# Optimization experiments

Measured on AMD Instinct MI355X. Metric: run time of the kernel, lower is better.

## Reference

```python
import jax, jax.numpy as jnp
import numpy as np
import math

D_MODEL = 1024
N_HEADS = 16
D_HEAD = D_MODEL // N_HEADS


def layer_norm(x, gamma, beta, eps=1e-5):
    mu = jnp.mean(x, axis=-1, keepdims=True)
    var = jnp.var(x, axis=-1, keepdims=True)
    return (x - mu) / jnp.sqrt(var + eps) * gamma + beta


def setup_inputs() -> dict:
    key = jax.random.key(0)
    ks = jax.random.split(key, 12)
    B, T, d = 4, 2048, D_MODEL
    s = 0.02
    x = jax.random.normal(ks[0], (B, T, d), dtype=jnp.float32)
    t = jnp.arange(B * T, dtype=jnp.float32).reshape(B, T) % T  # continuous positions
    return {
        "x": x,
        "t": t,
        "w_qkv": jax.random.normal(ks[1], (d, 3 * d), dtype=jnp.float32) * s,
        "b_qkv": jnp.zeros((3 * d,), jnp.float32),
        "w_proj": jax.random.normal(ks[2], (d, d), dtype=jnp.float32) * s,
        "b_proj": jnp.zeros((d,), jnp.float32),
        "g1": jnp.ones((d,), jnp.float32),
        "beta1": jnp.zeros((d,), jnp.float32),
        "g2": jnp.ones((d,), jnp.float32),
        "beta2": jnp.zeros((d,), jnp.float32),
        "w_mlp1": jax.random.normal(ks[3], (d, 4 * d), dtype=jnp.float32) * s,
        "b_mlp1": jnp.zeros((4 * d,), jnp.float32),
        "w_mlp2": jax.random.normal(ks[4], (4 * d, d), dtype=jnp.float32) * s,
        "b_mlp2": jnp.zeros((d,), jnp.float32),
    }


def reference(x, t, w_qkv, b_qkv, w_proj, b_proj, g1, beta1, g2, beta2, w_mlp1, b_mlp1, w_mlp2, b_mlp2):
    B, T, d = x.shape
    H, dh = N_HEADS, D_HEAD
    scale = dh ** -0.5

    h = layer_norm(x, g1, beta1)
    qkv = h @ w_qkv + b_qkv  # [B,T,3d]
    q, k, v = jnp.split(qkv, 3, axis=-1)
    # [B,T,H,dh] -> [B,H,T,dh]
    q = q.reshape(B, T, H, dh).transpose(0, 2, 1, 3)
    k = k.reshape(B, T, H, dh).transpose(0, 2, 1, 3)
    v = v.reshape(B, T, H, dh).transpose(0, 2, 1, 3)

    # ContinuousRoPE on d_head
    half = dh // 2
    freqs = jnp.exp(jnp.arange(half, dtype=jnp.float32) * (-math.log(10000.0) / (half - 1)))
    args = t[:, :, None] * freqs  # [B,T,half]
    cos = jnp.tile(jnp.cos(args), (1, 1, 2))[:, None]  # [B,1,T,dh]
    sin = jnp.tile(jnp.sin(args), (1, 1, 2))[:, None]

    def rotate_half(u):
        u1, u2 = u[..., :dh // 2], u[..., dh // 2:]
        return jnp.concatenate((-u2, u1), axis=-1)

    q = q * cos + rotate_half(q) * sin
    k = k * cos + rotate_half(k) * sin

    attn = jnp.einsum("bhqd,bhkd->bhqk", q, k) * scale  # [B,H,T,T]
    causal = jnp.tril(jnp.ones((T, T), dtype=bool))
    attn = jnp.where(causal, attn, -jnp.inf)
    attn = jax.nn.softmax(attn, axis=-1)
    o = jnp.einsum("bhqk,bhkd->bhqd", attn, v)  # [B,H,T,dh]
    o = o.transpose(0, 2, 1, 3).reshape(B, T, d)

    x1 = o @ w_proj + b_proj + x
    h2 = layer_norm(x1, g2, beta2)
    mlp = jax.nn.gelu(h2 @ w_mlp1 + b_mlp1, approximate=False) @ w_mlp2 + b_mlp2
    return x1 + mlp
```

## Files before the change

kernel.cpp:

```cpp
#include <hip/hip_runtime.h>

typedef __bf16  bf16x8 __attribute__((ext_vector_type(8)));
typedef float   f32x4  __attribute__((ext_vector_type(4)));

typedef const __attribute__((address_space(1))) void* gas_p;
typedef __attribute__((address_space(3))) void*       las_p;

__device__ __forceinline__ void glds16(const void* g, void* l) {
  __builtin_amdgcn_global_load_lds((gas_p)g, (las_p)l, 16, 0, 0);
}

__device__ __forceinline__ ushort f2bf(float f) {
  unsigned u = __float_as_uint(f);
  u += 0x7fffu + ((u >> 16) & 1u);
  return (ushort)(u >> 16);
}

__global__ __launch_bounds__(256) void castT_k(const float* __restrict__ w,
                                               ushort* __restrict__ wT,
                                               const int Kd, const int Nd) {
  __shared__ float t[32][33];
  const int nb = blockIdx.x * 32, kb = blockIdx.y * 32;
  const int tx = threadIdx.x & 31, ty = threadIdx.x >> 5;
#pragma unroll
  for (int r = 0; r < 32; r += 8)
    t[ty + r][tx] = w[(size_t)(kb + ty + r) * Nd + nb + tx];
  __syncthreads();
#pragma unroll
  for (int r = 0; r < 32; r += 8)
    wT[(size_t)(nb + ty + r) * Kd + kb + tx] = f2bf(t[tx][ty + r]);
}

__global__ __launch_bounds__(256) void ln_k(const float* __restrict__ x,
                                            const float* __restrict__ gam,
                                            const float* __restrict__ bet,
                                            ushort* __restrict__ out) {
  const int row = blockIdx.x, tid = threadIdx.x;
  const float4 v = ((const float4*)(x + (size_t)row * 1024))[tid];
  float s  = v.x + v.y + v.z + v.w;
  float sq = v.x * v.x + v.y * v.y + v.z * v.z + v.w * v.w;
#pragma unroll
  for (int o = 32; o > 0; o >>= 1) { s += __shfl_xor(s, o); sq += __shfl_xor(sq, o); }
  __shared__ float red[8];
  const int wid = tid >> 6, lane = tid & 63;
  if (lane == 0) { red[wid] = s; red[4 + wid] = sq; }
  __syncthreads();
  s  = red[0] + red[1] + red[2] + red[3];
  sq = red[4] + red[5] + red[6] + red[7];
  const float mu   = s * (1.0f / 1024.0f);
  const float var  = sq * (1.0f / 1024.0f) - mu * mu;
  const float rstd = rsqrtf(var + 1e-5f);
  const float4 gv = ((const float4*)gam)[tid];
  const float4 bv = ((const float4*)bet)[tid];
  ushort4 o4;
  o4.x = f2bf((v.x - mu) * rstd * gv.x + bv.x);
  o4.y = f2bf((v.y - mu) * rstd * gv.y + bv.y);
  o4.z = f2bf((v.z - mu) * rstd * gv.z + bv.z);
  o4.w = f2bf((v.w - mu) * rstd * gv.w + bv.w);
  ((ushort4*)(out + (size_t)row * 1024))[tid] = o4;
}

__global__ __launch_bounds__(256) void vtrans_k(const ushort* __restrict__ Vn,
                                                ushort* __restrict__ Vt) {
  const int bh = blockIdx.y, i0 = blockIdx.x * 64, tid = threadIdx.x;
  __shared__ ushort t[64][65];
  const ushort* src = Vn + (size_t)bh * (2048 * 64);
#pragma unroll
  for (int kk = 0; kk < 16; ++kk) {
    const int e = tid + kk * 256, r = e >> 6, c = e & 63;
    t[r][c] = src[(size_t)(i0 + r) * 64 + c];
  }
  __syncthreads();
  ushort* dst = Vt + (size_t)bh * (64 * 2048);
#pragma unroll
  for (int kk = 0; kk < 16; ++kk) {
    const int e = tid + kk * 256, r = e >> 6, c = e & 63;
    dst[(size_t)r * 2048 + i0 + c] = t[c][r];
  }
}

template <int EPI>
__global__ __launch_bounds__(256) void gemm_k(
    const ushort* __restrict__ A, const ushort* __restrict__ Bt,
    const int M, const int N, const int K,
    const float* __restrict__ bias,
    const float* __restrict__ resid,
    float* __restrict__ outf,
    ushort* __restrict__ outb,
    ushort* __restrict__ qo, ushort* __restrict__ ko, ushort* __restrict__ vo) {
  __shared__ ushort lA[2][128 * 32];
  __shared__ ushort lB[2][128 * 32];
  const int tid = threadIdx.x;
  const int wid = tid >> 6, lane = tid & 63;
  const int l15 = lane & 15, g = lane >> 4;
  const int m0 = blockIdx.y * 128, n0 = blockIdx.x * 128;
  const int wm = wid >> 1, wn = wid & 1;

  const int srow = wid * 16 + (lane >> 2);
  const int scol = (lane & 3) * 8;
  const ushort* Ag0 = A + (size_t)(m0 + srow) * K + scol;
  const ushort* Ag1 = Ag0 + (size_t)64 * K;
  const ushort* Bg0 = Bt + (size_t)(n0 + srow) * K + scol;
  const ushort* Bg1 = Bg0 + (size_t)64 * K;

  f32x4 acc[4][4] = {};

  const int nk = K >> 5;
  int cur = 0;
  glds16(Ag0, &lA[0][wid * 512]);
  glds16(Ag1, &lA[0][(wid + 4) * 512]);
  glds16(Bg0, &lB[0][wid * 512]);
  glds16(Bg1, &lB[0][(wid + 4) * 512]);

  for (int t = 0; t < nk; ++t) {
    __syncthreads();
    if (t + 1 < nk) {
      const int kt = (t + 1) << 5;
      const int nb = cur ^ 1;
      glds16(Ag0 + kt, &lA[nb][wid * 512]);
      glds16(Ag1 + kt, &lA[nb][(wid + 4) * 512]);
      glds16(Bg0 + kt, &lB[nb][wid * 512]);
      glds16(Bg1 + kt, &lB[nb][(wid + 4) * 512]);
    }
    const ushort* lar = &lA[cur][(wm * 64 + l15) * 32 + g * 8];
    const ushort* lbr = &lB[cur][(wn * 64 + l15) * 32 + g * 8];
    bf16x8 af[4], bfr[4];
#pragma unroll
    for (int m = 0; m < 4; ++m) af[m] = *(const bf16x8*)(lar + m * 16 * 32);
#pragma unroll
    for (int n = 0; n < 4; ++n) bfr[n] = *(const bf16x8*)(lbr + n * 16 * 32);
#pragma unroll
    for (int m = 0; m < 4; ++m)
#pragma unroll
      for (int n = 0; n < 4; ++n)
        acc[m][n] = __builtin_amdgcn_mfma_f32_16x16x32_bf16(af[m], bfr[n], acc[m][n], 0, 0, 0);
    cur ^= 1;
  }

  const int rb = m0 + wm * 64;
  const int cb = n0 + wn * 64;
  if constexpr (EPI == 0) {
#pragma unroll
    for (int m = 0; m < 4; ++m)
#pragma unroll
      for (int r = 0; r < 4; ++r) {
        const int s = rb + m * 16 + g * 4 + r;
        const int bb = s >> 11, ii = s & 2047;
#pragma unroll
        for (int n = 0; n < 2; ++n) {
          const int c = cb + n * 16 + l15;
          const int which = c >> 10, h = (c >> 6) & 15, dd = c & 63;
          const float vlo = acc[m][n][r] + bias[c];
          const float vhi = acc[m][n + 2][r] + bias[c + 32];
          const size_t off = ((size_t)((bb * 16 + h) * 2048 + ii)) * 64;
          if (which == 2) {
            vo[off + dd]      = f2bf(vlo);
            vo[off + dd + 32] = f2bf(vhi);
          } else {
            const float fr = __expf(-0.29710776f * (float)dd);
            const float ang = (float)ii * fr;
            const float c0 = cosf(ang), s0 = sinf(ang);
            float rlo = vlo * c0 - vhi * s0;
            float rhi = vhi * c0 + vlo * s0;
            if (which == 0) { rlo *= 0.125f; rhi *= 0.125f; }
            ushort* dst = (which == 0) ? qo : ko;
            dst[off + dd]      = f2bf(rlo);
            dst[off + dd + 32] = f2bf(rhi);
          }
        }
      }
  } else {
#pragma unroll
    for (int m = 0; m < 4; ++m)
#pragma unroll
      for (int n = 0; n < 4; ++n)
#pragma unroll
        for (int r = 0; r < 4; ++r) {
          const int row = rb + m * 16 + g * 4 + r;
          const int col = cb + n * 16 + l15;
          float v = acc[m][n][r] + bias[col];
          if constexpr (EPI == 1) {
            v += resid[(size_t)row * N + col];
            outf[(size_t)row * N + col] = v;
          } else {
            const float ge = 0.5f * v * (1.0f + erff(v * 0.70710678f));
            outb[(size_t)row * N + col] = f2bf(ge);
          }
        }
  }
}

__global__ __launch_bounds__(256) void attn_k(const ushort* __restrict__ Q,
                                              const ushort* __restrict__ K,
                                              const ushort* __restrict__ Vt,
                                              ushort* __restrict__ O) {
  const int bh = blockIdx.x;
  const int qt = 31 - blockIdx.y;
  const int tid = threadIdx.x, wid = tid >> 6, lane = tid & 63;
  const int l15 = lane & 15, g = lane >> 4;
  const size_t bho = (size_t)bh * (2048 * 64);
  const ushort* Qb = Q + bho;
  const char*   KbB = (const char*)(K + bho);
  const char*   VbB = (const char*)(Vt + bho);
  const int b = bh >> 4, h = bh & 15;

  __shared__ ushort kl[2][64 * 64];
  __shared__ ushort vl[2][64 * 64];
  __shared__ ushort pl[4][16 * 64];

  const int rbase = wid * 16;
  const int rsub  = lane >> 3;
  const int cbyte = (lane & 7) << 4;
  const int scb   = cbyte ^ (rsub << 4);

  const int q0 = qt * 64 + wid * 16;

  const bf16x8 qf0 = *(const bf16x8*)&Qb[(size_t)(q0 + l15) * 64 + g * 8];
  const bf16x8 qf1 = *(const bf16x8*)&Qb[(size_t)(q0 + l15) * 64 + 32 + g * 8];

  f32x4 o[4] = {};
  float m = -1e30f, l = 0.f;

  char* pbase = (char*)pl[wid];
  const int swz  = (l15 & 7) << 4;
  const int skey = (l15 & 7) << 4;

  const int nkt = qt + 1;

  {
    const char* ks0 = KbB + (size_t)(0 + rbase + rsub) * 128 + scb;
    const char* vs0 = VbB + (size_t)(rbase + rsub) * 4096 + scb;
    glds16(ks0,            (char*)kl[0] + rbase * 128);
    glds16(ks0 + 8 * 128,  (char*)kl[0] + (rbase + 8) * 128);
    glds16(vs0,            (char*)vl[0] + rbase * 128);
    glds16(vs0 + 8 * 4096, (char*)vl[0] + (rbase + 8) * 128);
  }
  int cur = 0;

  for (int kt = 0; kt < nkt; ++kt) {
    const int k0 = kt * 64;
    __syncthreads();
    if (kt + 1 < nkt) {
      const int nb = cur ^ 1, k1 = k0 + 64;
      const char* ks0 = KbB + (size_t)(k1 + rbase + rsub) * 128 + scb;
      const char* vs0 = VbB + (size_t)(rbase + rsub) * 4096 + (size_t)k1 * 2 + scb;
      glds16(ks0,            (char*)kl[nb] + rbase * 128);
      glds16(ks0 + 8 * 128,  (char*)kl[nb] + (rbase + 8) * 128);
      glds16(vs0,            (char*)vl[nb] + rbase * 128);
      glds16(vs0 + 8 * 4096, (char*)vl[nb] + (rbase + 8) * 128);
    }
    const char* Klds = (const char*)kl[cur];
    const char* Vlds = (const char*)vl[cur];

    f32x4 st[4];
    __builtin_amdgcn_s_setprio(1);
#pragma unroll
    for (int sub = 0; sub < 4; ++sub) {
      const int kr = sub * 16 + l15;
      const bf16x8 kf0 = *(const bf16x8*)(Klds + kr * 128 + ((g * 16) ^ skey));
      const bf16x8 kf1 = *(const bf16x8*)(Klds + kr * 128 + ((64 + g * 16) ^ skey));
      f32x4 z = {0.f, 0.f, 0.f, 0.f};
      f32x4 sv = __builtin_amdgcn_mfma_f32_16x16x32_bf16(kf0, qf0, z, 0, 0, 0);
      sv = __builtin_amdgcn_mfma_f32_16x16x32_bf16(kf1, qf1, sv, 0, 0, 0);
      st[sub] = sv;
    }
    __builtin_amdgcn_s_setprio(0);
    if (k0 + 63 > q0) {
#pragma unroll
      for (int sub = 0; sub < 4; ++sub) {
        const int kk = k0 + sub * 16 + g * 4;
#pragma unroll
        for (int r = 0; r < 4; ++r)
          if (kk + r > q0 + l15) st[sub][r] = -1e30f;
      }
    }
    f32x4 mv = st[0];
#pragma unroll
    for (int sub = 1; sub < 4; ++sub)
#pragma unroll
      for (int r = 0; r < 4; ++r) mv[r] = fmaxf(mv[r], st[sub][r]);
    float tm = fmaxf(fmaxf(mv[0], mv[1]), fmaxf(mv[2], mv[3]));
    tm = fmaxf(tm, __shfl_xor(tm, 16));
    tm = fmaxf(tm, __shfl_xor(tm, 32));
    if (!__all(tm - m <= 8.0f)) {
      const float mnew = fmaxf(m, tm);
      const float corr = __expf(m - mnew);
      m = mnew;
      l *= corr;
      float cr[4];
#pragma unroll
      for (int r = 0; r < 4; ++r) cr[r] = __shfl(corr, g * 4 + r);
#pragma unroll
      for (int nf = 0; nf < 4; ++nf)
#pragma unroll
        for (int r = 0; r < 4; ++r) o[nf][r] *= cr[r];
    }
    float ps = 0.f;
#pragma unroll
    for (int sub = 0; sub < 4; ++sub) {
      const float p0 = __expf(st[sub][0] - m);
      const float p1 = __expf(st[sub][1] - m);
      const float p2 = __expf(st[sub][2] - m);
      const float p3 = __expf(st[sub][3] - m);
      ps += (p0 + p1) + (p2 + p3);
      ushort4 pk;
      pk.x = f2bf(p0); pk.y = f2bf(p1); pk.z = f2bf(p2); pk.w = f2bf(p3);
      *(ushort4*)(pbase + ((l15 * 128 + ((sub * 32 + g * 8) ^ swz)))) = pk;
    }
    ps += __shfl_xor(ps, 16);
    ps += __shfl_xor(ps, 32);
    l += ps;
    const bf16x8 pf0 = *(const bf16x8*)(pbase + (l15 * 128 + ((g * 16) ^ swz)));
    const bf16x8 pf1 = *(const bf16x8*)(pbase + (l15 * 128 + ((64 + g * 16) ^ swz)));
    __builtin_amdgcn_s_setprio(1);
#pragma unroll
    for (int nf = 0; nf < 4; ++nf) {
      const int dr = nf * 16 + l15;
      const bf16x8 vf0 = *(const bf16x8*)(Vlds + dr * 128 + ((g * 16) ^ skey));
      const bf16x8 vf1 = *(const bf16x8*)(Vlds + dr * 128 + ((64 + g * 16) ^ skey));
      o[nf] = __builtin_amdgcn_mfma_f32_16x16x32_bf16(pf0, vf0, o[nf], 0, 0, 0);
      o[nf] = __builtin_amdgcn_mfma_f32_16x16x32_bf16(pf1, vf1, o[nf], 0, 0, 0);
    }
    __builtin_amdgcn_s_setprio(0);
    cur ^= 1;
  }
  const float linv = 1.0f / l;
  float li[4];
#pragma unroll
  for (int r = 0; r < 4; ++r) li[r] = __shfl(linv, g * 4 + r);
#pragma unroll
  for (int nf = 0; nf < 4; ++nf)
#pragma unroll
    for (int r = 0; r < 4; ++r) {
      const int qr = q0 + g * 4 + r;
      O[((size_t)(b * 2048 + qr)) * 1024 + h * 64 + nf * 16 + l15] = f2bf(o[nf][r] * li[r]);
    }
}

extern "C" void kernel_launch(void* const* d_in, const int* in_sizes, int n_in,
                              void* d_out, int out_size, void* d_ws, size_t ws_size,
                              hipStream_t stream) {
  const float* x      = (const float*)d_in[0];
  const float* w_qkv  = (const float*)d_in[2];
  const float* b_qkv  = (const float*)d_in[3];
  const float* w_proj = (const float*)d_in[4];
  const float* b_proj = (const float*)d_in[5];
  const float* g1     = (const float*)d_in[6];
  const float* be1    = (const float*)d_in[7];
  const float* g2     = (const float*)d_in[8];
  const float* be2    = (const float*)d_in[9];
  const float* w_mlp1 = (const float*)d_in[10];
  const float* b_mlp1 = (const float*)d_in[11];
  const float* w_mlp2 = (const float*)d_in[12];
  const float* b_mlp2 = (const float*)d_in[13];

  char* ws = (char*)d_ws;
  ushort* WQKVT  = (ushort*)(ws + 0);
  ushort* WPROJT = (ushort*)(ws + 6291456);
  ushort* WMLP1T = (ushort*)(ws + 8388608);
  ushort* WMLP2T = (ushort*)(ws + 16777216);
  ushort* H      = (ushort*)(ws + 25165824);
  ushort* Qs     = (ushort*)(ws + 41943040);
  ushort* Ks     = (ushort*)(ws + 58720256);
  ushort* Vn     = (ushort*)(ws + 75497472);
  ushort* Vt     = (ushort*)(ws + 92274688);
  ushort* M1     = (ushort*)(ws + 41943040);
  float*  X1     = (float*)(ws + 109051904);

  castT_k<<<dim3(3072 / 32, 1024 / 32), 256, 0, stream>>>(w_qkv, WQKVT, 1024, 3072);
  castT_k<<<dim3(1024 / 32, 1024 / 32), 256, 0, stream>>>(w_proj, WPROJT, 1024, 1024);
  castT_k<<<dim3(4096 / 32, 1024 / 32), 256, 0, stream>>>(w_mlp1, WMLP1T, 1024, 4096);
  castT_k<<<dim3(1024 / 32, 4096 / 32), 256, 0, stream>>>(w_mlp2, WMLP2T, 4096, 1024);

  ln_k<<<8192, 256, 0, stream>>>(x, g1, be1, H);

  gemm_k<0><<<dim3(3072 / 128, 8192 / 128), 256, 0, stream>>>(
      H, WQKVT, 8192, 3072, 1024, b_qkv, nullptr, nullptr, nullptr, Qs, Ks, Vn);

  vtrans_k<<<dim3(32, 64), 256, 0, stream>>>(Vn, Vt);

  attn_k<<<dim3(64, 32), 256, 0, stream>>>(Qs, Ks, Vt, H );

  gemm_k<1><<<dim3(1024 / 128, 8192 / 128), 256, 0, stream>>>(
      H, WPROJT, 8192, 1024, 1024, b_proj, x, X1, nullptr, nullptr, nullptr, nullptr);

  ln_k<<<8192, 256, 0, stream>>>(X1, g2, be2, H );

  gemm_k<2><<<dim3(4096 / 128, 8192 / 128), 256, 0, stream>>>(
      H, WMLP1T, 8192, 4096, 1024, b_mlp1, nullptr, nullptr, M1, nullptr, nullptr, nullptr);

  gemm_k<1><<<dim3(1024 / 128, 8192 / 128), 256, 0, stream>>>(
      M1, WMLP2T, 8192, 1024, 4096, b_mlp2, X1, (float*)d_out, nullptr, nullptr, nullptr, nullptr);
}
```

Measured before the change: 569.9 us.

## Replace GEMM with 256-wide tiled, 8-wave, swizzled, finer-pipelined kernel

```diff
diff --git a/kernel.cpp b/kernel.cpp
--- a/kernel.cpp
+++ b/kernel.cpp
@@ -15,6 +15,13 @@
   u += 0x7fffu + ((u >> 16) & 1u);
   return (ushort)(u >> 16);
 }
+
+__device__ __forceinline__ void barx() {
+  asm volatile("" ::: "memory");
+  __builtin_amdgcn_s_barrier();
+  asm volatile("" ::: "memory");
+}
+#define WAITVM(N) asm volatile("s_waitcnt vmcnt(" #N ")" ::: "memory")
 
 __global__ __launch_bounds__(256) void castT_k(const float* __restrict__ w,
                                                ushort* __restrict__ wT,
@@ -79,8 +86,8 @@
   }
 }
 
-template <int EPI>
-__global__ __launch_bounds__(256) void gemm_k(
+template <int MF, int EPI>
+__global__ __launch_bounds__(512, 2) void gemm2_k(
     const ushort* __restrict__ A, const ushort* __restrict__ Bt,
     const int M, const int N, const int K,
     const float* __restrict__ bias,
@@ -88,60 +95,104 @@
     float* __restrict__ outf,
     ushort* __restrict__ outb,
     ushort* __restrict__ qo, ushort* __restrict__ ko, ushort* __restrict__ vo) {
-  __shared__ ushort lA[2][128 * 32];
-  __shared__ ushort lB[2][128 * 32];
-  const int tid = threadIdx.x;
-  const int wid = tid >> 6, lane = tid & 63;
+  constexpr int BM = MF * 32;
+  constexpr int GA = MF / 4;
+  extern __shared__ ushort lds_u[];
+  ushort* aL = lds_u;
+  ushort* bL = lds_u + 4 * BM * 32;
+
+  const int tid = threadIdx.x, wid = tid >> 6, lane = tid & 63;
   const int l15 = lane & 15, g = lane >> 4;
-  const int m0 = blockIdx.y * 128, n0 = blockIdx.x * 128;
-  const int wm = wid >> 1, wn = wid & 1;
-
-  const int srow = wid * 16 + (lane >> 2);
-  const int scol = (lane & 3) * 8;
-  const ushort* Ag0 = A + (size_t)(m0 + srow) * K + scol;
-  const ushort* Ag1 = Ag0 + (size_t)64 * K;
-  const ushort* Bg0 = Bt + (size_t)(n0 + srow) * K + scol;
-  const ushort* Bg1 = Bg0 + (size_t)64 * K;
-
-  f32x4 acc[4][4] = {};
-
-  const int nk = K >> 5;
+  const int wr = wid >> 2, wc = wid & 3;
+  const int m0 = blockIdx.y * BM, n0 = blockIdx.x * 256;
+
+  const int srl = lane >> 2;
+  const int scb = ((lane & 3) << 4) ^ (((lane >> 3) & 3) << 4);
+  const int rk  = ((l15 >> 1) & 3) << 4;
+  const size_t Krow = (size_t)K * 2;
+
+  auto stageA = [&](int b, int kh, int t) {
+#pragma unroll
+    for (int L = 0; L < GA; ++L) {
+      const char* src = (const char*)A + (size_t)(m0 + L * 128 + wid * 16 + srl) * Krow
+                        + (size_t)t * 128 + kh * 64 + scb;
+      glds16(src, (char*)aL + (size_t)((b * 2 + kh) * BM + L * 128 + wid * 16) * 64);
+    }
+  };
+  auto stageB = [&](int b, int kh, int t) {
+#pragma unroll
+    for (int L = 0; L < 2; ++L) {
+      const char* src = (const char*)Bt + (size_t)(n0 + L * 128 + wid * 16 + srl) * Krow
+                        + (size_t)t * 128 + kh * 64 + scb;
+      glds16(src, (char*)bL + (size_t)((b * 2 + kh) * 256 + L * 128 + wid * 16) * 64);
+    }
+  };
+
+  bf16x8 af[MF], bfr[4];
+  f32x4 acc[MF][4] = {};
+
+  auto loadA = [&](int b, int kh) {
+#pragma unroll
+    for (int m = 0; m < MF; ++m)
+      af[m] = *(const bf16x8*)((const char*)aL +
+          (size_t)((b * 2 + kh) * BM + wr * (BM / 2) + m * 16 + l15) * 64 + ((g * 16) ^ rk));
+  };
+  auto loadB = [&](int b, int kh, int nh) {
+#pragma unroll
+    for (int n = 0; n < 2; ++n)
+      bfr[nh * 2 + n] = *(const bf16x8*)((const char*)bL +
+          (size_t)((b * 2 + kh) * 256 + wc * 64 + (nh * 2 + n) * 16 + l15) * 64 + ((g * 16) ^ rk));
+  };
+  auto mfma8 = [&](int nh) {
+    __builtin_amdgcn_s_setprio(1);
+#pragma unroll
+    for (int m = 0; m < MF; ++m) {
+      acc[m][nh * 2]     = __builtin_amdgcn_mfma_f32_16x16x32_bf16(af[m], bfr[nh * 2],     acc[m][nh * 2],     0, 0, 0);
+      acc[m][nh * 2 + 1] = __builtin_amdgcn_mfma_f32_16x16x32_bf16(af[m], bfr[nh * 2 + 1], acc[m][nh * 2 + 1], 0, 0, 0);
+    }
+    __builtin_amdgcn_s_setprio(0);
+  };
+
+  stageA(0, 0, 0); stageB(0, 0, 0); stageA(0, 1, 0); stageB(0, 1, 0);
+  if constexpr (MF == 8) { WAITVM(4); } else { WAITVM(3); }
+  barx();
+
+  const int nk = K >> 6;
   int cur = 0;
-  glds16(Ag0, &lA[0][wid * 512]);
-  glds16(Ag1, &lA[0][(wid + 4) * 512]);
-  glds16(Bg0, &lB[0][wid * 512]);
-  glds16(Bg1, &lB[0][(wid + 4) * 512]);
-
   for (int t = 0; t < nk; ++t) {
-    __syncthreads();
-    if (t + 1 < nk) {
-      const int kt = (t + 1) << 5;
-      const int nb = cur ^ 1;
-      glds16(Ag0 + kt, &lA[nb][wid * 512]);
-      glds16(Ag1 + kt, &lA[nb][(wid + 4) * 512]);
-      glds16(Bg0 + kt, &lB[nb][wid * 512]);
-      glds16(Bg1 + kt, &lB[nb][(wid + 4) * 512]);
-    }
-    const ushort* lar = &lA[cur][(wm * 64 + l15) * 32 + g * 8];
-    const ushort* lbr = &lB[cur][(wn * 64 + l15) * 32 + g * 8];
-    bf16x8 af[4], bfr[4];
-#pragma unroll
-    for (int m = 0; m < 4; ++m) af[m] = *(const bf16x8*)(lar + m * 16 * 32);
-#pragma unroll
-    for (int n = 0; n < 4; ++n) bfr[n] = *(const bf16x8*)(lbr + n * 16 * 32);
-#pragma unroll
-    for (int m = 0; m < 4; ++m)
-#pragma unroll
-      for (int n = 0; n < 4; ++n)
-        acc[m][n] = __builtin_amdgcn_mfma_f32_16x16x32_bf16(af[m], bfr[n], acc[m][n], 0, 0, 0);
-    cur ^= 1;
-  }
-
-  const int rb = m0 + wm * 64;
-  const int cb = n0 + wn * 64;
+    const bool pf = (t + 1 < nk);
+    const int nb = cur ^ 1;
+    loadA(cur, 0); loadB(cur, 0, 0);
+    if (pf) stageA(nb, 0, t + 1);
+    barx();
+    mfma8(0);
+    barx();
+    loadB(cur, 0, 1);
+    if (pf) stageB(nb, 0, t + 1);
+    barx();
+    mfma8(1);
+    if (pf) { if constexpr (MF == 8) { WAITVM(4); } else { WAITVM(3); } }
+    else    { WAITVM(0); }
+    barx();
+    loadA(cur, 1); loadB(cur, 1, 0);
+    if (pf) stageA(nb, 1, t + 1);
+    barx();
+    mfma8(0);
+    barx();
+    loadB(cur, 1, 1);
+    if (pf) stageB(nb, 1, t + 1);
+    barx();
+    mfma8(1);
+    if (pf) { if constexpr (MF == 8) { WAITVM(4); } else { WAITVM(3); } }
+    barx();
+    cur = nb;
+  }
+
+  const int rb = m0 + wr * (BM / 2);
+  const int cb = n0 + wc * 64;
   if constexpr (EPI == 0) {
 #pragma unroll
-    for (int m = 0; m < 4; ++m)
+    for (int m = 0; m < MF; ++m)
 #pragma unroll
       for (int r = 0; r < 4; ++r) {
         const int s = rb + m * 16 + g * 4 + r;
@@ -171,7 +222,7 @@
       }
   } else {
 #pragma unroll
-    for (int m = 0; m < 4; ++m)
+    for (int m = 0; m < MF; ++m)
 #pragma unroll
       for (int n = 0; n < 4; ++n)
 #pragma unroll
@@ -226,7 +277,6 @@
   const int skey = (l15 & 7) << 4;
 
   const int nkt = qt + 1;
-
   {
     const char* ks0 = KbB + (size_t)(0 + rbase + rsub) * 128 + scb;
     const char* vs0 = VbB + (size_t)(rbase + rsub) * 4096 + scb;
@@ -367,6 +417,10 @@
   ushort* M1     = (ushort*)(ws + 41943040);
   float*  X1     = (float*)(ws + 109051904);
 
+  hipFuncSetAttribute((const void*)gemm2_k<8, 0>, hipFuncAttributeMaxDynamicSharedMemorySize, 131072);
+  hipFuncSetAttribute((const void*)gemm2_k<8, 2>, hipFuncAttributeMaxDynamicSharedMemorySize, 131072);
+  hipFuncSetAttribute((const void*)gemm2_k<4, 1>, hipFuncAttributeMaxDynamicSharedMemorySize, 98304);
+
   castT_k<<<dim3(3072 / 32, 1024 / 32), 256, 0, stream>>>(w_qkv, WQKVT, 1024, 3072);
   castT_k<<<dim3(1024 / 32, 1024 / 32), 256, 0, stream>>>(w_proj, WPROJT, 1024, 1024);
   castT_k<<<dim3(4096 / 32, 1024 / 32), 256, 0, stream>>>(w_mlp1, WMLP1T, 1024, 4096);
@@ -374,21 +428,21 @@
 
   ln_k<<<8192, 256, 0, stream>>>(x, g1, be1, H);
 
-  gemm_k<0><<<dim3(3072 / 128, 8192 / 128), 256, 0, stream>>>(
+  gemm2_k<8, 0><<<dim3(3072 / 256, 8192 / 256), 512, 131072, stream>>>(
       H, WQKVT, 8192, 3072, 1024, b_qkv, nullptr, nullptr, nullptr, Qs, Ks, Vn);
 
   vtrans_k<<<dim3(32, 64), 256, 0, stream>>>(Vn, Vt);
 
   attn_k<<<dim3(64, 32), 256, 0, stream>>>(Qs, Ks, Vt, H );
 
-  gemm_k<1><<<dim3(1024 / 128, 8192 / 128), 256, 0, stream>>>(
+  gemm2_k<4, 1><<<dim3(1024 / 256, 8192 / 128), 512, 98304, stream>>>(
       H, WPROJT, 8192, 1024, 1024, b_proj, x, X1, nullptr, nullptr, nullptr, nullptr);
 
   ln_k<<<8192, 256, 0, stream>>>(X1, g2, be2, H );
 
-  gemm_k<2><<<dim3(4096 / 128, 8192 / 128), 256, 0, stream>>>(
+  gemm2_k<8, 2><<<dim3(4096 / 256, 8192 / 256), 512, 131072, stream>>>(
       H, WMLP1T, 8192, 4096, 1024, b_mlp1, nullptr, nullptr, M1, nullptr, nullptr, nullptr);
 
-  gemm_k<1><<<dim3(1024 / 128, 8192 / 128), 256, 0, stream>>>(
+  gemm2_k<4, 1><<<dim3(1024 / 256, 8192 / 128), 512, 98304, stream>>>(
       M1, WMLP2T, 8192, 1024, 4096, b_mlp2, X1, (float*)d_out, nullptr, nullptr, nullptr, nullptr);
 }
```

Measured after the change: 600.4 us. 5.3% more time.
